# Performance work log

Measured on AMD Instinct MI355X. Metric: run time of the kernel, lower is better.

## Reference

```python
import jax, jax.numpy as jnp
import numpy as np

NUM_BASES = 8


def setup_inputs() -> dict:
    key = jax.random.key(0)
    ks = jax.random.split(key, 8)
    N, E = 100000, 1600000
    IN_F, OUT_F, NUM_RELS = 128, 128, 16
    si = IN_F // NUM_BASES   # 16
    so = OUT_F // NUM_BASES  # 16
    return {
        "h": jax.random.normal(ks[0], (N, IN_F), dtype=jnp.float32),
        "norm": jax.random.uniform(ks[1], (N, 1), dtype=jnp.float32),
        "edge_src": jax.random.randint(ks[2], (E,), 0, N, dtype=jnp.int32),
        "edge_dst": jax.random.randint(ks[3], (E,), 0, N, dtype=jnp.int32),
        "edge_type": jax.random.randint(ks[4], (E,), 0, NUM_RELS, dtype=jnp.int32),
        "weight": jax.random.normal(ks[5], (NUM_RELS, NUM_BASES * si * so), dtype=jnp.float32) * 0.1,
        "bias_param": jax.random.normal(ks[6], (OUT_F,), dtype=jnp.float32) * 0.1,
        "loop_weight": jax.random.normal(ks[7], (IN_F, OUT_F), dtype=jnp.float32) * 0.1,
    }


def reference(h, norm, edge_src, edge_dst, edge_type, weight, bias_param, loop_weight):
    N, in_feat = h.shape
    out_feat = loop_weight.shape[1]
    si = in_feat // NUM_BASES
    so = out_feat // NUM_BASES
    E = edge_type.shape[0]

    # self-loop message (dropout=0.0 -> identity)
    loop_message = h @ loop_weight                      # [N, out_feat]

    # msg_func: gather per-edge relation weight blocks and do block-diag bmm
    W = weight[edge_type].reshape(E, NUM_BASES, si, so)  # [E, B, si, so]
    src = h[edge_src].reshape(E, NUM_BASES, si)          # [E, B, si]
    msg = jnp.einsum("ebi,ebio->ebo", src, W).reshape(E, out_feat)

    # scatter-sum messages to destination nodes, rescale by norm
    agg = jax.ops.segment_sum(msg, edge_dst, num_segments=N)  # [N, out_feat]
    node_repr = agg * norm

    # bias + self-loop + activation
    node_repr = node_repr + bias_param + loop_message
    return jax.nn.relu(node_repr)
```

## Files before the change

### kernel.cpp

```cpp
#include <hip/hip_runtime.h>


__device__ __forceinline__ unsigned int f2bf(float f) {
  const unsigned int u = __float_as_uint(f);
  return (u + 0x7FFFu + ((u >> 16) & 1u)) >> 16;
}

__global__ __launch_bounds__(256) void rgcn_init_kernel(
    const float* __restrict__ h, const float* __restrict__ loop_w,
    const float* __restrict__ bias, float* __restrict__ out, int N) {
  __shared__ float lw[128 * 128];
  for (int idx = threadIdx.x; idx < 128 * 128 / 4; idx += 256) {
    ((float4*)lw)[idx] = ((const float4*)loop_w)[idx];
  }
  __syncthreads();

  const int lane = threadIdx.x & 63;
  const int wid = threadIdx.x >> 6;
  const int group0 = blockIdx.x * 4 + wid;
  const int ngroups = gridDim.x * 4;
  const int totgroups = (N + 3) >> 2;
  const float b0 = bias[lane];
  const float b1 = bias[64 + lane];

  for (int g = group0; g < totgroups; g += ngroups) {
    const int n0 = g * 4;
    const int nn = (N - n0 < 4) ? (N - n0) : 4;
    if (nn == 4) {
      const float* __restrict__ r0 = h + (size_t)n0 * 128;
      const float* __restrict__ r1 = r0 + 128;
      const float* __restrict__ r2 = r1 + 128;
      const float* __restrict__ r3 = r2 + 128;
      float a00 = b0, a01 = b1, a10 = b0, a11 = b1;
      float a20 = b0, a21 = b1, a30 = b0, a31 = b1;
#pragma unroll 4
      for (int k = 0; k < 128; ++k) {
        const float w0 = lw[k * 128 + lane];
        const float w1 = lw[k * 128 + 64 + lane];
        a00 = fmaf(r0[k], w0, a00); a01 = fmaf(r0[k], w1, a01);
        a10 = fmaf(r1[k], w0, a10); a11 = fmaf(r1[k], w1, a11);
        a20 = fmaf(r2[k], w0, a20); a21 = fmaf(r2[k], w1, a21);
        a30 = fmaf(r3[k], w0, a30); a31 = fmaf(r3[k], w1, a31);
      }
      float* __restrict__ o0 = out + (size_t)n0 * 128;
      o0[lane] = a00;        o0[64 + lane] = a01;
      o0[128 + lane] = a10;  o0[192 + lane] = a11;
      o0[256 + lane] = a20;  o0[320 + lane] = a21;
      o0[384 + lane] = a30;  o0[448 + lane] = a31;
    } else {
      for (int r = 0; r < nn; ++r) {
        const int n = n0 + r;
        const float* __restrict__ hr = h + (size_t)n * 128;
        float a0 = b0, a1 = b1;
#pragma unroll 4
        for (int k = 0; k < 128; ++k) {
          const float a = hr[k];
          a0 = fmaf(a, lw[k * 128 + lane], a0);
          a1 = fmaf(a, lw[k * 128 + 64 + lane], a1);
        }
        out[(size_t)n * 128 + lane] = a0;
        out[(size_t)n * 128 + 64 + lane] = a1;
      }
    }
  }
}

__global__ __launch_bounds__(1024) void rgcn_precompute_kernel(
    const float* __restrict__ h, const float* __restrict__ weight,
    unsigned int* __restrict__ M, int base, int cend) {
  const int lane = threadIdx.x & 63;
  const int t = threadIdx.x >> 6;
  const int b = lane >> 4;
  const int o = lane & 15;

  const float* __restrict__ wb = weight + t * 2048 + b * 256 + o;
  float wlo[16], whi[16];
#pragma unroll
  for (int i = 0; i < 16; ++i) {
    wlo[i] = wb[i * 16];
    whi[i] = wb[1024 + i * 16];
  }

  const int span = cend - base;
  const int n0 = base + (int)(((long)blockIdx.x * span) / gridDim.x);
  const int n1 = base + (int)(((long)(blockIdx.x + 1) * span) / gridDim.x);

  for (int n = n0; n < n1; ++n) {
    const float4* __restrict__ hp =
        (const float4*)(h + (size_t)n * 128) + (b << 2);
    const float4 x0 = hp[0], x1 = hp[1], x2 = hp[2], x3 = hp[3];
    const float4 y0 = hp[16], y1 = hp[17], y2 = hp[18], y3 = hp[19];

    float a0 = x0.x * wlo[0], a1 = x0.y * wlo[1];
    a0 = fmaf(x0.z, wlo[2], a0);  a1 = fmaf(x0.w, wlo[3], a1);
    a0 = fmaf(x1.x, wlo[4], a0);  a1 = fmaf(x1.y, wlo[5], a1);
    a0 = fmaf(x1.z, wlo[6], a0);  a1 = fmaf(x1.w, wlo[7], a1);
    a0 = fmaf(x2.x, wlo[8], a0);  a1 = fmaf(x2.y, wlo[9], a1);
    a0 = fmaf(x2.z, wlo[10], a0); a1 = fmaf(x2.w, wlo[11], a1);
    a0 = fmaf(x3.x, wlo[12], a0); a1 = fmaf(x3.y, wlo[13], a1);
    a0 = fmaf(x3.z, wlo[14], a0); a1 = fmaf(x3.w, wlo[15], a1);

    float c0 = y0.x * whi[0], c1 = y0.y * whi[1];
    c0 = fmaf(y0.z, whi[2], c0);  c1 = fmaf(y0.w, whi[3], c1);
    c0 = fmaf(y1.x, whi[4], c0);  c1 = fmaf(y1.y, whi[5], c1);
    c0 = fmaf(y1.z, whi[6], c0);  c1 = fmaf(y1.w, whi[7], c1);
    c0 = fmaf(y2.x, whi[8], c0);  c1 = fmaf(y2.y, whi[9], c1);
    c0 = fmaf(y2.z, whi[10], c0); c1 = fmaf(y2.w, whi[11], c1);
    c0 = fmaf(y3.x, whi[12], c0); c1 = fmaf(y3.y, whi[13], c1);
    c0 = fmaf(y3.z, whi[14], c0); c1 = fmaf(y3.w, whi[15], c1);

    const unsigned int pk = f2bf(a0 + a1) | (f2bf(c0 + c1) << 16);
    M[(((size_t)(n - base) << 4) | t) * 64 + lane] = pk;
  }
}

__global__ __launch_bounds__(256) void rgcn_zero_kernel(int* __restrict__ p,
                                                        int n) {
  for (int i = blockIdx.x * 256 + threadIdx.x; i < n; i += gridDim.x * 256)
    p[i] = 0;
}

__global__ __launch_bounds__(256) void rgcn_hist_kernel(
    const int* __restrict__ esrc, const int* __restrict__ edst,
    int* __restrict__ cnt, int E, int N, unsigned S) {
  for (int e = blockIdx.x * 256 + threadIdx.x; e < E; e += gridDim.x * 256) {
    const unsigned q = (unsigned)esrc[e] / S;
    atomicAdd(&cnt[(int)(q * (unsigned)N) + edst[e]], 1);
  }
}

__global__ __launch_bounds__(1024) void rgcn_scan_pass1(
    const int* __restrict__ cnt, int* __restrict__ partial, int bins) {
  __shared__ int sums[1024];
  const int t = threadIdx.x;
  const int base = blockIdx.x * 4096 + t * 4;
  int s = 0;
  if (base + 3 < bins) {
    const int4 v = *(const int4*)(cnt + base);
    s = v.x + v.y + v.z + v.w;
  } else {
    for (int j = 0; j < 4; ++j)
      if (base + j < bins) s += cnt[base + j];
  }
  sums[t] = s;
  __syncthreads();
  for (int off = 512; off > 0; off >>= 1) {
    if (t < off) sums[t] += sums[t + off];
    __syncthreads();
  }
  if (t == 0) partial[blockIdx.x] = sums[0];
}

__global__ __launch_bounds__(1024) void rgcn_scan_pass2(
    int* __restrict__ partial, int nb) {
  __shared__ int sc[1024];
  const int t = threadIdx.x;
  int v[4];
  int s = 0;
#pragma unroll
  for (int j = 0; j < 4; ++j) {
    const int i = t * 4 + j;
    v[j] = (i < nb) ? partial[i] : 0;
    s += v[j];
  }
  sc[t] = s;
  __syncthreads();
#pragma unroll
  for (int off = 1; off < 1024; off <<= 1) {
    const int add = (t >= off) ? sc[t - off] : 0;
    __syncthreads();
    sc[t] += add;
    __syncthreads();
  }
  int run = (t == 0) ? 0 : sc[t - 1];
#pragma unroll
  for (int j = 0; j < 4; ++j) {
    const int i = t * 4 + j;
    if (i < nb) partial[i] = run;
    run += v[j];
  }
}

__global__ __launch_bounds__(1024) void rgcn_scan_pass3(
    const int* __restrict__ cnt, const int* __restrict__ partial,
    int* __restrict__ row_ptr, int* __restrict__ cursor, int bins) {
  __shared__ int sums[1024];
  const int t = threadIdx.x;
  const int base = blockIdx.x * 4096 + t * 4;
  int v0 = 0, v1 = 0, v2 = 0, v3 = 0;
  if (base + 3 < bins) {
    const int4 v = *(const int4*)(cnt + base);
    v0 = v.x; v1 = v.y; v2 = v.z; v3 = v.w;
  } else {
    if (base < bins) v0 = cnt[base];
    if (base + 1 < bins) v1 = cnt[base + 1];
    if (base + 2 < bins) v2 = cnt[base + 2];
  }
  sums[t] = v0 + v1 + v2 + v3;
  __syncthreads();
#pragma unroll
  for (int off = 1; off < 1024; off <<= 1) {
    const int add = (t >= off) ? sums[t - off] : 0;
    __syncthreads();
    sums[t] += add;
    __syncthreads();
  }
  const int run = partial[blockIdx.x] + ((t == 0) ? 0 : sums[t - 1]);
  const int p0 = run, p1 = p0 + v0, p2 = p1 + v1, p3 = p2 + v2;
  if (base + 3 < bins) {
    *(int4*)(row_ptr + base) = make_int4(p0, p1, p2, p3);
    *(int4*)(cursor + base) = make_int4(p0, p1, p2, p3);
  } else {
    if (base < bins) { row_ptr[base] = p0; cursor[base] = p0; }
    if (base + 1 < bins) { row_ptr[base + 1] = p1; cursor[base + 1] = p1; }
    if (base + 2 < bins) { row_ptr[base + 2] = p2; cursor[base + 2] = p2; }
  }
}

__global__ void rgcn_set_kernel(int* __restrict__ p, int v) {
  if (threadIdx.x == 0) *p = v;
}

__global__ __launch_bounds__(256) void rgcn_scatter_kernel(
    const int* __restrict__ esrc, const int* __restrict__ edst,
    const int* __restrict__ etype, int* __restrict__ cursor,
    int* __restrict__ srec, int E, int N, unsigned S) {
  for (int e = blockIdx.x * 256 + threadIdx.x; e < E; e += gridDim.x * 256) {
    const unsigned s = (unsigned)esrc[e];
    const unsigned q = s / S;
    const int key = (int)(q * (unsigned)N) + edst[e];
    const int p = atomicAdd(&cursor[key], 1);
    srec[p] = (int)((s - q * S) << 4) | etype[e];
  }
}

__global__ __launch_bounds__(256) void rgcn_gather3_kernel(
    const float* __restrict__ norm, const int* __restrict__ srec,
    const int* __restrict__ rpc, const unsigned int* __restrict__ M,
    float* __restrict__ out, int N, int final_pass) {
  const int lane = threadIdx.x & 63;
  const int w0 = blockIdx.x * 4 + (threadIdx.x >> 6);
  const int nw = gridDim.x * 4;

  for (int d = w0; d < N; d += nw) {
    const int e0 = rpc[d];
    const int e1 = rpc[d + 1];
    if (!final_pass && e0 == e1) continue;

    float acc0 = 0.f, acc1 = 0.f;
    int e = e0;
    for (; e + 8 <= e1; e += 8) {
      const int r0 = srec[e], r1 = srec[e + 1], r2 = srec[e + 2],
                r3 = srec[e + 3], r4 = srec[e + 4], r5 = srec[e + 5],
                r6 = srec[e + 6], r7 = srec[e + 7];
      const unsigned int v0 = M[(size_t)r0 * 64 + lane];
      const unsigned int v1 = M[(size_t)r1 * 64 + lane];
      const unsigned int v2 = M[(size_t)r2 * 64 + lane];
      const unsigned int v3 = M[(size_t)r3 * 64 + lane];
      const unsigned int v4 = M[(size_t)r4 * 64 + lane];
      const unsigned int v5 = M[(size_t)r5 * 64 + lane];
      const unsigned int v6 = M[(size_t)r6 * 64 + lane];
      const unsigned int v7 = M[(size_t)r7 * 64 + lane];
      acc0 += __uint_as_float(v0 << 16);
      acc1 += __uint_as_float(v0 & 0xFFFF0000u);
      acc0 += __uint_as_float(v1 << 16);
      acc1 += __uint_as_float(v1 & 0xFFFF0000u);
      acc0 += __uint_as_float(v2 << 16);
      acc1 += __uint_as_float(v2 & 0xFFFF0000u);
      acc0 += __uint_as_float(v3 << 16);
      acc1 += __uint_as_float(v3 & 0xFFFF0000u);
      acc0 += __uint_as_float(v4 << 16);
      acc1 += __uint_as_float(v4 & 0xFFFF0000u);
      acc0 += __uint_as_float(v5 << 16);
      acc1 += __uint_as_float(v5 & 0xFFFF0000u);
      acc0 += __uint_as_float(v6 << 16);
      acc1 += __uint_as_float(v6 & 0xFFFF0000u);
      acc0 += __uint_as_float(v7 << 16);
      acc1 += __uint_as_float(v7 & 0xFFFF0000u);
    }
    for (; e + 4 <= e1; e += 4) {
      const int r0 = srec[e], r1 = srec[e + 1], r2 = srec[e + 2],
                r3 = srec[e + 3];
      const unsigned int v0 = M[(size_t)r0 * 64 + lane];
      const unsigned int v1 = M[(size_t)r1 * 64 + lane];
      const unsigned int v2 = M[(size_t)r2 * 64 + lane];
      const unsigned int v3 = M[(size_t)r3 * 64 + lane];
      acc0 += __uint_as_float(v0 << 16);
      acc1 += __uint_as_float(v0 & 0xFFFF0000u);
      acc0 += __uint_as_float(v1 << 16);
      acc1 += __uint_as_float(v1 & 0xFFFF0000u);
      acc0 += __uint_as_float(v2 << 16);
      acc1 += __uint_as_float(v2 & 0xFFFF0000u);
      acc0 += __uint_as_float(v3 << 16);
      acc1 += __uint_as_float(v3 & 0xFFFF0000u);
    }
    for (; e < e1; ++e) {
      const unsigned int v = M[(size_t)srec[e] * 64 + lane];
      acc0 += __uint_as_float(v << 16);
      acc1 += __uint_as_float(v & 0xFFFF0000u);
    }

    const float nm = norm[d];
    float* __restrict__ op = out + ((size_t)d << 7);
    float o0 = fmaf(acc0, nm, op[lane]);
    float o1 = fmaf(acc1, nm, op[64 + lane]);
    if (final_pass) {
      o0 = fmaxf(o0, 0.f);
      o1 = fmaxf(o1, 0.f);
    }
    op[lane] = o0;
    op[64 + lane] = o1;
  }
}

__global__ __launch_bounds__(256) void rgcn_edge_kernel(
    const float* __restrict__ h, const float* __restrict__ norm,
    const int* __restrict__ esrc, const int* __restrict__ edst,
    const int* __restrict__ etype, const float* __restrict__ weight,
    float* __restrict__ out, int E) {
  const int lane = threadIdx.x & 63;
  const int wid = threadIdx.x >> 6;
  const int wave0 = blockIdx.x * 4 + wid;
  const int nwaves = gridDim.x * 4;
  const int b = lane >> 4;
  const int o = lane & 15;

  for (int e = wave0; e < E; e += nwaves) {
    const int src = esrc[e];
    const int dst = edst[e];
    const int et = etype[e];
    const float s_lo = h[src * 128 + lane];
    const float s_hi = h[src * 128 + 64 + lane];
    const float nrm = norm[dst];
    const float* __restrict__ Wb = weight + et * 2048 + b * 256 + o;
    float m0 = 0.f, m1 = 0.f;
#pragma unroll
    for (int i = 0; i < 16; ++i) {
      const float a_lo = __shfl(s_lo, (lane & 48) + i, 64);
      const float a_hi = __shfl(s_hi, (lane & 48) + i, 64);
      m0 = fmaf(a_lo, Wb[i * 16], m0);
      m1 = fmaf(a_hi, Wb[1024 + i * 16], m1);
    }
    atomicAdd(&out[dst * 128 + lane], m0 * nrm);
    atomicAdd(&out[dst * 128 + 64 + lane], m1 * nrm);
  }
}

__global__ __launch_bounds__(256) void rgcn_relu_kernel(float* __restrict__ out,
                                                        int total4) {
  int i = blockIdx.x * 256 + threadIdx.x;
  const int stride = gridDim.x * 256;
  for (; i < total4; i += stride) {
    float4 v = ((float4*)out)[i];
    v.x = fmaxf(v.x, 0.f);
    v.y = fmaxf(v.y, 0.f);
    v.z = fmaxf(v.z, 0.f);
    v.w = fmaxf(v.w, 0.f);
    ((float4*)out)[i] = v;
  }
}

extern "C" void kernel_launch(void* const* d_in, const int* in_sizes, int n_in,
                              void* d_out, int out_size, void* d_ws, size_t ws_size,
                              hipStream_t stream) {
  const float* h      = (const float*)d_in[0];
  const float* norm   = (const float*)d_in[1];
  const int*   esrc   = (const int*)d_in[2];
  const int*   edst   = (const int*)d_in[3];
  const int*   etype  = (const int*)d_in[4];
  const float* weight = (const float*)d_in[5];
  const float* bias   = (const float*)d_in[6];
  const float* loop_w = (const float*)d_in[7];
  float* out = (float*)d_out;

  const int N = in_sizes[0] / 128;
  const int E = in_sizes[2];
  const int nrels = in_sizes[5] / 2048;

  rgcn_init_kernel<<<2048, 256, 0, stream>>>(h, loop_w, bias, out, N);

  int C = -1, S = 0;
  size_t ofs_rp = 0, ofs_cur = 0, ofs_part = 0, ofs_srec = 0, ofs_M = 0;
  if (nrels == 16 && N >= 1 && N < (1 << 26)) {
    for (int cc = 1; cc <= 64; ++cc) {
      const size_t bins = (size_t)cc * (size_t)N;
      if (bins > (size_t)4096 * 4096) break;
      const int ss = (N + cc - 1) / cc;
      const size_t o_rp = (bins + 3) & ~(size_t)3;
      const size_t o_cur = (o_rp + bins + 1 + 3) & ~(size_t)3;
      const size_t o_part = (o_cur + bins + 3) & ~(size_t)3;
      const size_t o_srec = o_part + 4096;
      const size_t o_M = (o_srec + (size_t)E + 15) & ~(size_t)15;
      const size_t need = (o_M + (size_t)ss * 16 * 64) * 4;
      if (need <= ws_size) {
        C = cc; S = ss;
        ofs_rp = o_rp; ofs_cur = o_cur; ofs_part = o_part;
        ofs_srec = o_srec; ofs_M = o_M;
        break;
      }
    }
  }

  if (C >= 1) {
    const int bins = C * N;
    const int nb = (bins + 4095) / 4096;
    int* base    = (int*)d_ws;
    int* cnt     = base;
    int* row_ptr = base + ofs_rp;
    int* cursor  = base + ofs_cur;
    int* partial = base + ofs_part;
    int* srec    = base + ofs_srec;
    unsigned int* M = (unsigned int*)(base + ofs_M);

    rgcn_zero_kernel<<<1024, 256, 0, stream>>>(cnt, bins);
    rgcn_hist_kernel<<<2048, 256, 0, stream>>>(esrc, edst, cnt, E, N,
                                               (unsigned)S);
    rgcn_scan_pass1<<<nb, 1024, 0, stream>>>(cnt, partial, bins);
    rgcn_scan_pass2<<<1, 1024, 0, stream>>>(partial, nb);
    rgcn_scan_pass3<<<nb, 1024, 0, stream>>>(cnt, partial, row_ptr, cursor,
                                             bins);
    rgcn_set_kernel<<<1, 64, 0, stream>>>(row_ptr + bins, E);
    rgcn_scatter_kernel<<<2048, 256, 0, stream>>>(esrc, edst, etype, cursor,
                                                  srec, E, N, (unsigned)S);
    for (int c = 0; c < C; ++c) {
      const int cbase = c * S;
      const int cend = (cbase + S < N) ? (cbase + S) : N;
      if (cbase >= N) break;
      rgcn_precompute_kernel<<<512, 1024, 0, stream>>>(h, weight, M, cbase,
                                                       cend);
      rgcn_gather3_kernel<<<2048, 256, 0, stream>>>(
          norm, srec, row_ptr + (size_t)c * N, M, out, N,
          (c == C - 1) ? 1 : 0);
    }
  } else {
    rgcn_edge_kernel<<<4096, 256, 0, stream>>>(h, norm, esrc, edst, etype,
                                               weight, out, E);
    rgcn_relu_kernel<<<2048, 256, 0, stream>>>(out, (N * 128) / 4);
  }
}
```

Measured before the change: 1.081 ms.

## Stage node features in double-buffered shared memory in precompute kernel

The per-relation precompute kernel now loads batches of 32 node feature rows cooperatively into a double-buffered LDS tile with coalesced float4 loads. It prefetches the next batch into registers while computing on the current one. Previously every wavefront read each h row redundantly from global memory. Work is distributed round-robin by batch instead of contiguous spans, which adds barrier overhead and 32KB of LDS per block that may limit occupancy.

```diff
diff --git a/kernel.cpp b/kernel.cpp
--- a/kernel.cpp
+++ b/kernel.cpp
@@ -1,5 +1,7 @@
 #include <hip/hip_runtime.h>
 
+
+#define NB 32
 
 __device__ __forceinline__ unsigned int f2bf(float f) {
   const unsigned int u = __float_as_uint(f);
@@ -68,10 +70,14 @@
 __global__ __launch_bounds__(1024) void rgcn_precompute_kernel(
     const float* __restrict__ h, const float* __restrict__ weight,
     unsigned int* __restrict__ M, int base, int cend) {
-  const int lane = threadIdx.x & 63;
-  const int t = threadIdx.x >> 6;
+  __shared__ float hs[2][NB * 128];
+  const int tid = threadIdx.x;
+  const int lane = tid & 63;
+  const int t = tid >> 6;
   const int b = lane >> 4;
   const int o = lane & 15;
+  const int snode = tid >> 5;
+  const int sc4 = tid & 31;
 
   const float* __restrict__ wb = weight + t * 2048 + b * 256 + o;
   float wlo[16], whi[16];
@@ -82,35 +88,65 @@
   }
 
   const int span = cend - base;
-  const int n0 = base + (int)(((long)blockIdx.x * span) / gridDim.x);
-  const int n1 = base + (int)(((long)(blockIdx.x + 1) * span) / gridDim.x);
-
-  for (int n = n0; n < n1; ++n) {
-    const float4* __restrict__ hp =
-        (const float4*)(h + (size_t)n * 128) + (b << 2);
-    const float4 x0 = hp[0], x1 = hp[1], x2 = hp[2], x3 = hp[3];
-    const float4 y0 = hp[16], y1 = hp[17], y2 = hp[18], y3 = hp[19];
-
-    float a0 = x0.x * wlo[0], a1 = x0.y * wlo[1];
-    a0 = fmaf(x0.z, wlo[2], a0);  a1 = fmaf(x0.w, wlo[3], a1);
-    a0 = fmaf(x1.x, wlo[4], a0);  a1 = fmaf(x1.y, wlo[5], a1);
-    a0 = fmaf(x1.z, wlo[6], a0);  a1 = fmaf(x1.w, wlo[7], a1);
-    a0 = fmaf(x2.x, wlo[8], a0);  a1 = fmaf(x2.y, wlo[9], a1);
-    a0 = fmaf(x2.z, wlo[10], a0); a1 = fmaf(x2.w, wlo[11], a1);
-    a0 = fmaf(x3.x, wlo[12], a0); a1 = fmaf(x3.y, wlo[13], a1);
-    a0 = fmaf(x3.z, wlo[14], a0); a1 = fmaf(x3.w, wlo[15], a1);
-
-    float c0 = y0.x * whi[0], c1 = y0.y * whi[1];
-    c0 = fmaf(y0.z, whi[2], c0);  c1 = fmaf(y0.w, whi[3], c1);
-    c0 = fmaf(y1.x, whi[4], c0);  c1 = fmaf(y1.y, whi[5], c1);
-    c0 = fmaf(y1.z, whi[6], c0);  c1 = fmaf(y1.w, whi[7], c1);
-    c0 = fmaf(y2.x, whi[8], c0);  c1 = fmaf(y2.y, whi[9], c1);
-    c0 = fmaf(y2.z, whi[10], c0); c1 = fmaf(y2.w, whi[11], c1);
-    c0 = fmaf(y3.x, whi[12], c0); c1 = fmaf(y3.y, whi[13], c1);
-    c0 = fmaf(y3.z, whi[14], c0); c1 = fmaf(y3.w, whi[15], c1);
-
-    const unsigned int pk = f2bf(a0 + a1) | (f2bf(c0 + c1) << 16);
-    M[(((size_t)(n - base) << 4) | t) * 64 + lane] = pk;
+  const int nbatches = (span + NB - 1) / NB;
+
+  int bt = blockIdx.x;
+  if (bt >= nbatches) return;
+  {
+    const int n = base + bt * NB + snode;
+    if (n < cend)
+      ((float4*)hs[0])[tid] =
+          *((const float4*)(h + (size_t)n * 128) + sc4);
+  }
+  __syncthreads();
+
+  int bufc = 0;
+  for (; bt < nbatches; bt += gridDim.x) {
+    const int btn = bt + gridDim.x;
+    float4 pf;
+    bool have = false;
+    if (btn < nbatches) {
+      const int n = base + btn * NB + snode;
+      if (n < cend) {
+        pf = *((const float4*)(h + (size_t)n * 128) + sc4);
+        have = true;
+      }
+    }
+
+    const int nb = base + bt * NB;
+    const int jmax = (cend - nb < NB) ? (cend - nb) : NB;
+    const float* __restrict__ bufp = hs[bufc];
+#pragma unroll 4
+    for (int j = 0; j < jmax; ++j) {
+      const float4* __restrict__ hl = (const float4*)(bufp + j * 128) + (b << 2);
+      const float4 x0 = hl[0], x1 = hl[1], x2 = hl[2], x3 = hl[3];
+      const float4 y0 = hl[16], y1 = hl[17], y2 = hl[18], y3 = hl[19];
+
+      float a0 = x0.x * wlo[0], a1 = x0.y * wlo[1];
+      a0 = fmaf(x0.z, wlo[2], a0);  a1 = fmaf(x0.w, wlo[3], a1);
+      a0 = fmaf(x1.x, wlo[4], a0);  a1 = fmaf(x1.y, wlo[5], a1);
+      a0 = fmaf(x1.z, wlo[6], a0);  a1 = fmaf(x1.w, wlo[7], a1);
+      a0 = fmaf(x2.x, wlo[8], a0);  a1 = fmaf(x2.y, wlo[9], a1);
+      a0 = fmaf(x2.z, wlo[10], a0); a1 = fmaf(x2.w, wlo[11], a1);
+      a0 = fmaf(x3.x, wlo[12], a0); a1 = fmaf(x3.y, wlo[13], a1);
+      a0 = fmaf(x3.z, wlo[14], a0); a1 = fmaf(x3.w, wlo[15], a1);
+
+      float c0 = y0.x * whi[0], c1 = y0.y * whi[1];
+      c0 = fmaf(y0.z, whi[2], c0);  c1 = fmaf(y0.w, whi[3], c1);
+      c0 = fmaf(y1.x, whi[4], c0);  c1 = fmaf(y1.y, whi[5], c1);
+      c0 = fmaf(y1.z, whi[6], c0);  c1 = fmaf(y1.w, whi[7], c1);
+      c0 = fmaf(y2.x, whi[8], c0);  c1 = fmaf(y2.y, whi[9], c1);
+      c0 = fmaf(y2.z, whi[10], c0); c1 = fmaf(y2.w, whi[11], c1);
+      c0 = fmaf(y3.x, whi[12], c0); c1 = fmaf(y3.y, whi[13], c1);
+      c0 = fmaf(y3.z, whi[14], c0); c1 = fmaf(y3.w, whi[15], c1);
+
+      const unsigned int pk = f2bf(a0 + a1) | (f2bf(c0 + c1) << 16);
+      M[(((size_t)(nb - base + j) << 4) | t) * 64 + lane] = pk;
+    }
+
+    if (have) ((float4*)hs[bufc ^ 1])[tid] = pf;
+    __syncthreads();
+    bufc ^= 1;
   }
 }
 
```

Result: slower. 1.404 ms (+29.9%).
